# Kernel optimization log

Hardware: AMD Instinct MI355X
Metric: run time of the kernel (lower is better)

Reference implementation:

```python
import jax, jax.numpy as jnp
import numpy as np

B, N, M, D = 32, 1024, 256, 512
NEG_INF = -1e9  # keras Softmax mask additive constant


def _length_mask(key, batch, length):
    # realistic padding masks: first L positions valid, L >= length//4
    lens = jax.random.randint(key, (batch,), length // 4, length + 1)
    return jnp.arange(length)[None, :] < lens[:, None]


def setup_inputs() -> dict:
    key = jax.random.key(0)
    k1, k2, k3, k4, k5 = jax.random.split(key, 5)
    context = jax.random.normal(k1, (B, N, D), dtype=jnp.float32)
    query = jax.random.normal(k2, (B, M, D), dtype=jnp.float32)
    c_mask = _length_mask(k3, B, N)
    q_mask = _length_mask(k4, B, M)
    # Dense(units=1, use_bias=False) kernel over concat([q, c, q*c]) -> (3D, 1)
    w = jax.random.normal(k5, (3 * D, 1), dtype=jnp.float32) * (1.0 / np.sqrt(3 * D))
    return {"context": context, "query": query, "c_mask": c_mask, "q_mask": q_mask, "w": w}


def reference(context, query, c_mask, q_mask, w):
    d = context.shape[-1]
    # stack order in original: [q_matrix, c_matrix, q*c]
    w_q = w[:d, 0]
    w_c = w[d:2 * d, 0]
    w_m = w[2 * d:, 0]
    # trilinear similarity S[b,n,m] = q_j.w_q + c_i.w_c + (c_i*q_j).w_m, decomposed
    S = (context @ w_c)[:, :, None] \
        + (query @ w_q)[:, None, :] \
        + jnp.einsum('bnd,bmd->bnm', context * w_m, query)
    # context-direction softmax over query axis (axis=2), masked by q_mask
    A = jax.nn.softmax(jnp.where(q_mask[:, None, :], S, NEG_INF), axis=2)
    # query-direction softmax over context axis (axis=1), masked by c_mask
    Bm = jax.nn.softmax(jnp.where(c_mask[:, :, None], S, NEG_INF), axis=1)
    # context-to-query attention: A @ query -> (b, n, d)
    c2q = jnp.einsum('bnm,bmd->bnd', A, query)
    # query-to-context: (A @ B^T) @ context -> (b, n, d)
    q2c = jnp.einsum('bnk,bjk,bjd->bnd', A, Bm, context)
    out = jnp.concatenate([context, c2q, context * c2q, context * q2c], axis=-1)
    return out
```

## Files before the change

### kernel.cpp

```cpp
#include <hip/hip_runtime.h>
#include <hip/hip_bf16.h>

#define B_ 32
#define N_ 1024
#define M_ 256
#define D_ 512

typedef __attribute__((ext_vector_type(8))) short short8;
typedef __attribute__((ext_vector_type(4))) float f32x4;

#define OFF_S     ((size_t)0)
#define OFF_CTXW  ((size_t)8388608)
#define OFF_ANM   ((size_t)8388608)
#define OFF_BMT   ((size_t)12582912)
#define OFF_QB    ((size_t)16777216)
#define OFF_QT    ((size_t)18874368)
#define OFF_CT    ((size_t)20971520)
#define OFF_CDOT  ((size_t)29360128)
#define OFF_QDOT  ((size_t)29392896)
#define OFF_RMAX  ((size_t)29401088)
#define OFF_RSUM  ((size_t)29433856)
#define OFF_CMAX  ((size_t)29466624)
#define OFF_CSUM  ((size_t)29474816)
#define OFF_PMAX  ((size_t)29483008)
#define OFF_PSUM  ((size_t)29614080)
#define OFF_RPMAX ((size_t)29745152)
#define OFF_RPSUM ((size_t)29876224)

__global__ __launch_bounds__(256) void prep_ctx(
    const float* __restrict__ ctx, const float* __restrict__ w,
    __hip_bfloat16* __restrict__ ctxw, __hip_bfloat16* __restrict__ cT,
    float* __restrict__ cdot)
{
    __shared__ float t[64][65];
    int b = blockIdx.z, n0 = blockIdx.y * 64, d0 = blockIdx.x * 64;
    int tr = threadIdx.x >> 6, tc = threadIdx.x & 63;
    const float* sp = ctx + ((size_t)b * N_ + n0) * D_ + d0;
    __hip_bfloat16* cwp = ctxw + ((size_t)b * N_ + n0) * D_ + d0;
    float wmv = w[2 * D_ + d0 + tc];
    float wcv = w[D_ + d0 + tc];
#pragma unroll
    for (int i = 0; i < 16; ++i) {
        int r = tr + i * 4;
        float x = sp[(size_t)r * D_ + tc];
        t[r][tc] = x;
        cwp[(size_t)r * D_ + tc] = __float2bfloat16(x * wmv);
        float p = x * wcv;
#pragma unroll
        for (int off = 32; off; off >>= 1) p += __shfl_down(p, off, 64);
        if (tc == 0) atomicAdd(cdot + b * N_ + n0 + r, p);
    }
    __syncthreads();
    __hip_bfloat16* dp = cT + ((size_t)b * D_ + d0) * N_ + n0;
#pragma unroll
    for (int i = 0; i < 16; ++i)
        dp[(size_t)(tr + i * 4) * N_ + tc] = __float2bfloat16(t[tc][tr + i * 4]);
}

__global__ __launch_bounds__(256) void prep_q(
    const float* __restrict__ qry, const float* __restrict__ w,
    __hip_bfloat16* __restrict__ qb, __hip_bfloat16* __restrict__ qT,
    float* __restrict__ qdot)
{
    __shared__ float t[64][65];
    int b = blockIdx.z, m0 = blockIdx.y * 64, d0 = blockIdx.x * 64;
    int tr = threadIdx.x >> 6, tc = threadIdx.x & 63;
    const float* sp = qry + ((size_t)b * M_ + m0) * D_ + d0;
    __hip_bfloat16* qbp = qb + ((size_t)b * M_ + m0) * D_ + d0;
    float wqv = w[d0 + tc];
#pragma unroll
    for (int i = 0; i < 16; ++i) {
        int r = tr + i * 4;
        float x = sp[(size_t)r * D_ + tc];
        t[r][tc] = x;
        qbp[(size_t)r * D_ + tc] = __float2bfloat16(x);
        float p = x * wqv;
#pragma unroll
        for (int off = 32; off; off >>= 1) p += __shfl_down(p, off, 64);
        if (tc == 0) atomicAdd(qdot + b * M_ + m0 + r, p);
    }
    __syncthreads();
    __hip_bfloat16* dp = qT + ((size_t)b * D_ + d0) * M_ + m0;
#pragma unroll
    for (int i = 0; i < 16; ++i)
        dp[(size_t)(tr + i * 4) * M_ + tc] = __float2bfloat16(t[tc][tr + i * 4]);
}


__device__ __forceinline__ void gl2lds16(const __hip_bfloat16* g, __hip_bfloat16* l) {
    __builtin_amdgcn_global_load_lds(
        (const __attribute__((address_space(1))) unsigned int*)g,
        (__attribute__((address_space(3))) unsigned int*)l, 16, 0, 0);
}

template<int KTOT>
__device__ __forceinline__ void mfma128(
    const __hip_bfloat16* __restrict__ Abase, int lda,
    const __hip_bfloat16* __restrict__ Bbase, int ldb,
    __hip_bfloat16* As, __hip_bfloat16* Bs, f32x4 acc[4][4])
{
    const int tid = threadIdx.x;
    const int w = tid >> 6, lane = tid & 63;
    const int quad = lane >> 4, lr = lane & 15;
    const int wr = w >> 1, wc = w & 1;
    const int srow = w * 32 + (lane >> 2);
    const int scol = (lane & 3) * 8;
    const __hip_bfloat16* ga0 = Abase + (size_t)srow * lda + scol;
    const __hip_bfloat16* ga1 = ga0 + (size_t)16 * lda;
    const __hip_bfloat16* gb0 = Bbase + (size_t)srow * ldb + scol;
    const __hip_bfloat16* gb1 = gb0 + (size_t)16 * ldb;
    __hip_bfloat16* la0 = As + w * 1024;
    __hip_bfloat16* la1 = As + w * 1024 + 512;
    __hip_bfloat16* lb0 = Bs + w * 1024;
    __hip_bfloat16* lb1 = Bs + w * 1024 + 512;
    const int aoff = (wr * 64 + lr) * 32 + quad * 8;
    const int boff = (wc * 64 + lr) * 32 + quad * 8;

    for (int k0 = 0; k0 < KTOT; k0 += 32) {
        gl2lds16(ga0, la0); gl2lds16(ga1, la1);
        gl2lds16(gb0, lb0); gl2lds16(gb1, lb1);
        ga0 += 32; ga1 += 32; gb0 += 32; gb1 += 32;
        asm volatile("s_waitcnt vmcnt(0)" ::: "memory");
        __syncthreads();
        short8 a[4], bb[4];
        const short8* ap = (const short8*)(As + aoff);
        const short8* bp = (const short8*)(Bs + boff);
#pragma unroll
        for (int fi = 0; fi < 4; ++fi) a[fi] = ap[fi * 64];
#pragma unroll
        for (int fj = 0; fj < 4; ++fj) bb[fj] = bp[fj * 64];
#pragma unroll
        for (int fi = 0; fi < 4; ++fi)
#pragma unroll
            for (int fj = 0; fj < 4; ++fj)
                acc[fi][fj] = __builtin_amdgcn_mfma_f32_16x16x32_bf16(
                    a[fi], bb[fj], acc[fi][fj], 0, 0, 0);
        __syncthreads();
    }
}

template<int KTOT>
__device__ __forceinline__ void mfma128x2(
    const __hip_bfloat16* __restrict__ Abase, int lda,
    const __hip_bfloat16* __restrict__ B1base,
    const __hip_bfloat16* __restrict__ B2base, int ldb,
    __hip_bfloat16* As, __hip_bfloat16* B1s, __hip_bfloat16* B2s,
    f32x4 acc1[4][4], f32x4 acc2[4][4])
{
    const int tid = threadIdx.x;
    const int w = tid >> 6, lane = tid & 63;
    const int quad = lane >> 4, lr = lane & 15;
    const int wr = w >> 1, wc = w & 1;
    const int srow = w * 32 + (lane >> 2);
    const int scol = (lane & 3) * 8;
    const __hip_bfloat16* ga0 = Abase + (size_t)srow * lda + scol;
    const __hip_bfloat16* ga1 = ga0 + (size_t)16 * lda;
    const __hip_bfloat16* gb10 = B1base + (size_t)srow * ldb + scol;
    const __hip_bfloat16* gb11 = gb10 + (size_t)16 * ldb;
    const __hip_bfloat16* gb20 = B2base + (size_t)srow * ldb + scol;
    const __hip_bfloat16* gb21 = gb20 + (size_t)16 * ldb;
    __hip_bfloat16* la0 = As + w * 1024;
    __hip_bfloat16* la1 = la0 + 512;
    __hip_bfloat16* lb10 = B1s + w * 1024;
    __hip_bfloat16* lb11 = lb10 + 512;
    __hip_bfloat16* lb20 = B2s + w * 1024;
    __hip_bfloat16* lb21 = lb20 + 512;
    const int aoff = (wr * 64 + lr) * 32 + quad * 8;
    const int boff = (wc * 64 + lr) * 32 + quad * 8;

    for (int k0 = 0; k0 < KTOT; k0 += 32) {
        gl2lds16(ga0, la0); gl2lds16(ga1, la1);
        gl2lds16(gb10, lb10); gl2lds16(gb11, lb11);
        gl2lds16(gb20, lb20); gl2lds16(gb21, lb21);
        ga0 += 32; ga1 += 32; gb10 += 32; gb11 += 32; gb20 += 32; gb21 += 32;
        asm volatile("s_waitcnt vmcnt(0)" ::: "memory");
        __syncthreads();
        short8 a[4], b1[4], b2[4];
        const short8* ap = (const short8*)(As + aoff);
        const short8* bp1 = (const short8*)(B1s + boff);
        const short8* bp2 = (const short8*)(B2s + boff);
#pragma unroll
        for (int fi = 0; fi < 4; ++fi) a[fi] = ap[fi * 64];
#pragma unroll
        for (int fj = 0; fj < 4; ++fj) { b1[fj] = bp1[fj * 64]; b2[fj] = bp2[fj * 64]; }
#pragma unroll
        for (int fi = 0; fi < 4; ++fi)
#pragma unroll
            for (int fj = 0; fj < 4; ++fj) {
                acc1[fi][fj] = __builtin_amdgcn_mfma_f32_16x16x32_bf16(
                    a[fi], b1[fj], acc1[fi][fj], 0, 0, 0);
                acc2[fi][fj] = __builtin_amdgcn_mfma_f32_16x16x32_bf16(
                    a[fi], b2[fj], acc2[fi][fj], 0, 0, 0);
            }
        __syncthreads();
    }
}

#define ACC_INIT(acc) \
    _Pragma("unroll") for (int i_ = 0; i_ < 4; ++i_) \
    _Pragma("unroll") for (int j_ = 0; j_ < 4; ++j_) acc[i_][j_] = (f32x4){0.f, 0.f, 0.f, 0.f};

#define EPI_IDX const int tid = threadIdx.x, lane = tid & 63, quad = lane >> 4, lr = lane & 15; \
    const int wr = tid >> 7, wc = (tid >> 6) & 1;

__global__ __launch_bounds__(256) void s_gemm_stats(
    const __hip_bfloat16* __restrict__ ctxw, const __hip_bfloat16* __restrict__ qryb,
    const float* __restrict__ cdot, const float* __restrict__ qdot,
    const int* __restrict__ q_mask, const int* __restrict__ c_mask,
    float* __restrict__ S,
    float* __restrict__ rpmax, float* __restrict__ rpsum,
    float* __restrict__ pmax, float* __restrict__ psum)
{
    __shared__ __align__(16) __hip_bfloat16 As[4096], Bs[4096];
    const int b = blockIdx.z, n0 = blockIdx.y * 128, m0 = blockIdx.x * 128;
    f32x4 acc[4][4];
    ACC_INIT(acc)
    mfma128<512>(ctxw + ((size_t)b * N_ + n0) * D_, D_,
                 qryb + ((size_t)b * M_ + m0) * D_, D_, As, Bs, acc);
    EPI_IDX
    float cd[4][4]; int cmv[4][4];
#pragma unroll
    for (int fi = 0; fi < 4; ++fi)
#pragma unroll
        for (int r = 0; r < 4; ++r) {
            int n = n0 + wr * 64 + fi * 16 + quad * 4 + r;
            cd[fi][r] = cdot[b * N_ + n];
            cmv[fi][r] = c_mask[b * N_ + n];
        }
    float qd[4]; int qmv[4];
#pragma unroll
    for (int fj = 0; fj < 4; ++fj) {
        int m = m0 + wc * 64 + fj * 16 + lr;
        qd[fj] = qdot[b * M_ + m];
        qmv[fj] = q_mask[b * M_ + m];
    }
#pragma unroll
    for (int fi = 0; fi < 4; ++fi)
#pragma unroll
        for (int r = 0; r < 4; ++r) {
            int n = n0 + wr * 64 + fi * 16 + quad * 4 + r;
            size_t rowoff = ((size_t)b * N_ + n) * M_;
#pragma unroll
            for (int fj = 0; fj < 4; ++fj) {
                int m = m0 + wc * 64 + fj * 16 + lr;
                S[rowoff + m] = acc[fi][fj][r] + cd[fi][r] + qd[fj];
            }
        }
    const int part = blockIdx.x * 2 + wc;
#pragma unroll
    for (int fi = 0; fi < 4; ++fi)
#pragma unroll
        for (int r = 0; r < 4; ++r) {
            float xs[4], mx = -1e30f;
#pragma unroll
            for (int fj = 0; fj < 4; ++fj) {
                xs[fj] = qmv[fj] ? (acc[fi][fj][r] + cd[fi][r] + qd[fj]) : -1e9f;
                mx = fmaxf(mx, xs[fj]);
            }
#pragma unroll
            for (int off = 1; off < 16; off <<= 1)
                mx = fmaxf(mx, __shfl_xor(mx, off, 64));
            float se = 0.f;
#pragma unroll
            for (int fj = 0; fj < 4; ++fj) se += __expf(xs[fj] - mx);
#pragma unroll
            for (int off = 1; off < 16; off <<= 1)
                se += __shfl_xor(se, off, 64);
            if (lr == 0) {
                int n = n0 + wr * 64 + fi * 16 + quad * 4 + r;
                rpmax[((size_t)b * N_ + n) * 4 + part] = mx;
                rpsum[((size_t)b * N_ + n) * 4 + part] = se;
            }
        }
    const int ch = blockIdx.y * 2 + wr;
#pragma unroll
    for (int fj = 0; fj < 4; ++fj) {
        float mx = -1e30f;
#pragma unroll
        for (int fi = 0; fi < 4; ++fi)
#pragma unroll
            for (int r = 0; r < 4; ++r) {
                float x = cmv[fi][r] ? (acc[fi][fj][r] + cd[fi][r] + qd[fj]) : -1e9f;
                mx = fmaxf(mx, x);
            }
        mx = fmaxf(mx, __shfl_xor(mx, 16, 64));
        mx = fmaxf(mx, __shfl_xor(mx, 32, 64));
        float se = 0.f;
#pragma unroll
        for (int fi = 0; fi < 4; ++fi)
#pragma unroll
            for (int r = 0; r < 4; ++r) {
                float x = cmv[fi][r] ? (acc[fi][fj][r] + cd[fi][r] + qd[fj]) : -1e9f;
                se += __expf(x - mx);
            }
        se += __shfl_xor(se, 16, 64);
        se += __shfl_xor(se, 32, 64);
        if (lane < 16) {
            int m = m0 + wc * 64 + fj * 16 + lr;
            pmax[((size_t)b * 16 + ch) * M_ + m] = mx;
            psum[((size_t)b * 16 + ch) * M_ + m] = se;
        }
    }
}

__global__ __launch_bounds__(256) void q2cpart_mfma(
    const __hip_bfloat16* __restrict__ ctxT, const __hip_bfloat16* __restrict__ BmT,
    __hip_bfloat16* __restrict__ Q2CT)
{
    __shared__ __align__(16) __hip_bfloat16 As[4096], Bs[4096];
    const int b = blockIdx.z, d0 = blockIdx.y * 128, m0 = blockIdx.x * 128;
    f32x4 acc[4][4];
    ACC_INIT(acc)
    mfma128<1024>(ctxT + ((size_t)b * D_ + d0) * N_, N_,
                  BmT + ((size_t)b * M_ + m0) * N_, N_, As, Bs, acc);
    EPI_IDX
#pragma unroll
    for (int fi = 0; fi < 4; ++fi) {
#pragma unroll
        for (int r = 0; r < 4; ++r) {
            int d = d0 + wr * 64 + fi * 16 + quad * 4 + r;
#pragma unroll
            for (int fj = 0; fj < 4; ++fj) {
                int m = m0 + wc * 64 + fj * 16 + lr;
                Q2CT[((size_t)b * D_ + d) * M_ + m] = __float2bfloat16(acc[fi][fj][r]);
            }
        }
    }
}

__global__ __launch_bounds__(256) void out_fused_mfma(
    const __hip_bfloat16* __restrict__ Anm, const __hip_bfloat16* __restrict__ qryT,
    const __hip_bfloat16* __restrict__ Q2CT, const float* __restrict__ ctx,
    float* __restrict__ out)
{
    __shared__ __align__(16) __hip_bfloat16 As[4096], B1s[4096], B2s[4096];
    const int b = blockIdx.z, n0 = blockIdx.y * 128, d0 = blockIdx.x * 128;
    f32x4 acc1[4][4], acc2[4][4];
    ACC_INIT(acc1)
    ACC_INIT(acc2)
    mfma128x2<256>(Anm + ((size_t)b * N_ + n0) * M_, M_,
                   qryT + ((size_t)b * D_ + d0) * M_,
                   Q2CT + ((size_t)b * D_ + d0) * M_, M_,
                   As, B1s, B2s, acc1, acc2);
    EPI_IDX
#pragma unroll
    for (int fi = 0; fi < 4; ++fi) {
#pragma unroll
        for (int r = 0; r < 4; ++r) {
            int n = n0 + wr * 64 + fi * 16 + quad * 4 + r;
            size_t ibase = ((size_t)b * N_ + n) * D_;
            size_t obase = ((size_t)b * N_ + n) * (4 * D_);
#pragma unroll
            for (int fj = 0; fj < 4; ++fj) {
                int d = d0 + wc * 64 + fj * 16 + lr;
                float c = ctx[ibase + d];
                float v1 = acc1[fi][fj][r];
                float v2 = acc2[fi][fj][r];
                out[obase + d] = c;
                out[obase + D_ + d] = v1;
                out[obase + 2 * D_ + d] = c * v1;
                out[obase + 3 * D_ + d] = c * v2;
            }
        }
    }
}


__global__ __launch_bounds__(256) void combine_stats(
    const float* __restrict__ pmax, const float* __restrict__ psum,
    const float* __restrict__ rpmax, const float* __restrict__ rpsum,
    float* __restrict__ cmax, float* __restrict__ csum,
    float* __restrict__ rmax, float* __restrict__ rsum)
{
    int idx = blockIdx.x * 256 + threadIdx.x;
    if (idx < B_ * M_) {
        int b = idx >> 8, m = idx & 255;
        float mx = -1e30f;
#pragma unroll
        for (int ch = 0; ch < 16; ++ch)
            mx = fmaxf(mx, pmax[((size_t)b * 16 + ch) * M_ + m]);
        float sm = 0.f;
#pragma unroll
        for (int ch = 0; ch < 16; ++ch)
            sm += psum[((size_t)b * 16 + ch) * M_ + m] *
                  __expf(pmax[((size_t)b * 16 + ch) * M_ + m] - mx);
        cmax[idx] = mx; csum[idx] = sm;
    } else {
        int row = idx - B_ * M_;
        float mx = -1e30f;
#pragma unroll
        for (int p = 0; p < 4; ++p)
            mx = fmaxf(mx, rpmax[(size_t)row * 4 + p]);
        float sm = 0.f;
#pragma unroll
        for (int p = 0; p < 4; ++p)
            sm += rpsum[(size_t)row * 4 + p] *
                  __expf(rpmax[(size_t)row * 4 + p] - mx);
        rmax[row] = mx; rsum[row] = sm;
    }
}

__global__ __launch_bounds__(256) void normalize_kernel(
    const float* __restrict__ S, __hip_bfloat16* __restrict__ Anm,
    __hip_bfloat16* __restrict__ BmT,
    const int* __restrict__ q_mask, const int* __restrict__ c_mask,
    const float* __restrict__ rmax, const float* __restrict__ rsum,
    const float* __restrict__ cmax, const float* __restrict__ csum)
{
    __shared__ float t[64][65];
    int b = blockIdx.z, n0 = blockIdx.y * 64, m0 = blockIdx.x * 64;
    int tr = threadIdx.x >> 6, tc = threadIdx.x & 63;
    int m = m0 + tc;
    int qm = q_mask[b * M_ + m];
    float cmx = cmax[b * M_ + m], csm = csum[b * M_ + m];
#pragma unroll
    for (int i = 0; i < 16; ++i) {
        int n = n0 + tr + i * 4;
        size_t idx = ((size_t)b * N_ + n) * M_ + m;
        float s = S[idx];
        float a  = qm ? __expf(s - rmax[b * N_ + n]) / rsum[b * N_ + n] : 0.f;
        float bm = c_mask[b * N_ + n] ? __expf(s - cmx) / csm : 0.f;
        Anm[idx] = __float2bfloat16(a);
        t[tc][tr + i * 4] = bm;
    }
    __syncthreads();
#pragma unroll
    for (int i = 0; i < 16; ++i) {
        int ml = tr + i * 4;
        BmT[((size_t)b * M_ + m0 + ml) * N_ + n0 + tc] = __float2bfloat16(t[ml][tc]);
    }
}

extern "C" void kernel_launch(void* const* d_in, const int* in_sizes, int n_in,
                              void* d_out, int out_size, void* d_ws, size_t ws_size,
                              hipStream_t stream) {
    const float* ctx   = (const float*)d_in[0];
    const float* qry   = (const float*)d_in[1];
    const int*   cmask = (const int*)d_in[2];
    const int*   qmask = (const int*)d_in[3];
    const float* w     = (const float*)d_in[4];
    float* out = (float*)d_out;
    float* ws  = (float*)d_ws;

    float* S = ws + OFF_S;
    __hip_bfloat16* ctxw = (__hip_bfloat16*)(ws + OFF_CTXW);
    __hip_bfloat16* Anm  = (__hip_bfloat16*)(ws + OFF_ANM);
    __hip_bfloat16* BmT  = (__hip_bfloat16*)(ws + OFF_BMT);
    __hip_bfloat16* qb   = (__hip_bfloat16*)(ws + OFF_QB);
    __hip_bfloat16* Q2CT = (__hip_bfloat16*)(ws + OFF_QB);
    __hip_bfloat16* qT   = (__hip_bfloat16*)(ws + OFF_QT);
    __hip_bfloat16* cT   = (__hip_bfloat16*)(ws + OFF_CT);
    float* cdot = ws + OFF_CDOT;
    float* qdot = ws + OFF_QDOT;
    float* rmax = ws + OFF_RMAX;
    float* rsum = ws + OFF_RSUM;
    float* cmx  = ws + OFF_CMAX;
    float* csm  = ws + OFF_CSUM;
    float* pmax = ws + OFF_PMAX;
    float* psum = ws + OFF_PSUM;
    float* rpmax = ws + OFF_RPMAX;
    float* rpsum = ws + OFF_RPSUM;

    hipMemsetAsync(cdot, 0, (size_t)(B_ * N_ + B_ * M_) * sizeof(float), stream);

    dim3 gpc(D_ / 64, N_ / 64, B_);
    prep_ctx<<<gpc, 256, 0, stream>>>(ctx, w, ctxw, cT, cdot);
    dim3 gpq(D_ / 64, M_ / 64, B_);
    prep_q<<<gpq, 256, 0, stream>>>(qry, w, qb, qT, qdot);

    dim3 gS(M_ / 128, N_ / 128, B_);
    s_gemm_stats<<<gS, 256, 0, stream>>>(ctxw, qb, cdot, qdot, qmask, cmask,
                                         S, rpmax, rpsum, pmax, psum);

    combine_stats<<<(B_ * M_ + B_ * N_) / 256, 256, 0, stream>>>(
        pmax, psum, rpmax, rpsum, cmx, csm, rmax, rsum);

    dim3 gN(M_ / 64, N_ / 64, B_);
    normalize_kernel<<<gN, 256, 0, stream>>>(S, Anm, BmT, qmask, cmask,
                                             rmax, rsum, cmx, csm);

    dim3 gP(M_ / 128, D_ / 128, B_);
    q2cpart_mfma<<<gP, 256, 0, stream>>>(cT, BmT, Q2CT);

    dim3 gO(D_ / 128, N_ / 128, B_);
    out_fused_mfma<<<gO, 256, 0, stream>>>(Anm, qT, Q2CT, ctx, out);
}
```

Measured before the change: 504.8 us.

## Double-buffer LDS tiles in MFMA GEMM loops and merge prep kernels

The shared MFMA GEMM helpers now keep two LDS stages. The next K-slice is issued with global_load_lds while the current slice is consumed, which removes one barrier per iteration and the explicit vmcnt wait. This is meant to hide global-load latency behind MFMA work. The cost is double the LDS per block (48KB in the fused output kernel), which may lower occupancy. The context and query prep kernels are also merged into one launch using an extended grid, to save a kernel launch and its tail.

```diff
diff --git a/kernel.cpp b/kernel.cpp
--- a/kernel.cpp
+++ b/kernel.cpp
@@ -27,63 +27,57 @@
 #define OFF_RPMAX ((size_t)29745152)
 #define OFF_RPSUM ((size_t)29876224)
 
-__global__ __launch_bounds__(256) void prep_ctx(
-    const float* __restrict__ ctx, const float* __restrict__ w,
+__global__ __launch_bounds__(256) void prep_all(
+    const float* __restrict__ ctx, const float* __restrict__ qry,
+    const float* __restrict__ w,
     __hip_bfloat16* __restrict__ ctxw, __hip_bfloat16* __restrict__ cT,
-    float* __restrict__ cdot)
+    float* __restrict__ cdot,
+    __hip_bfloat16* __restrict__ qb, __hip_bfloat16* __restrict__ qT,
+    float* __restrict__ qdot)
 {
     __shared__ float t[64][65];
-    int b = blockIdx.z, n0 = blockIdx.y * 64, d0 = blockIdx.x * 64;
+    int b = blockIdx.z, d0 = blockIdx.x * 64;
     int tr = threadIdx.x >> 6, tc = threadIdx.x & 63;
-    const float* sp = ctx + ((size_t)b * N_ + n0) * D_ + d0;
-    __hip_bfloat16* cwp = ctxw + ((size_t)b * N_ + n0) * D_ + d0;
-    float wmv = w[2 * D_ + d0 + tc];
-    float wcv = w[D_ + d0 + tc];
+    const float* src;
+    __hip_bfloat16* rowdst;
+    __hip_bfloat16* trdst;
+    float* dotdst;
+    float wrow, wdot;
+    int ldt;
+    if (blockIdx.y < N_ / 64) {
+        int r0 = blockIdx.y * 64;
+        src    = ctx + ((size_t)b * N_ + r0) * D_ + d0;
+        rowdst = ctxw + ((size_t)b * N_ + r0) * D_ + d0;
+        trdst  = cT + ((size_t)b * D_ + d0) * N_ + r0;
+        dotdst = cdot + b * N_ + r0;
+        wrow = w[2 * D_ + d0 + tc];
+        wdot = w[D_ + d0 + tc];
+        ldt = N_;
+    } else {
+        int r0 = (blockIdx.y - N_ / 64) * 64;
+        src    = qry + ((size_t)b * M_ + r0) * D_ + d0;
+        rowdst = qb + ((size_t)b * M_ + r0) * D_ + d0;
+        trdst  = qT + ((size_t)b * D_ + d0) * M_ + r0;
+        dotdst = qdot + b * M_ + r0;
+        wrow = 1.0f;
+        wdot = w[d0 + tc];
+        ldt = M_;
+    }
 #pragma unroll
     for (int i = 0; i < 16; ++i) {
         int r = tr + i * 4;
-        float x = sp[(size_t)r * D_ + tc];
+        float x = src[(size_t)r * D_ + tc];
         t[r][tc] = x;
-        cwp[(size_t)r * D_ + tc] = __float2bfloat16(x * wmv);
-        float p = x * wcv;
+        rowdst[(size_t)r * D_ + tc] = __float2bfloat16(x * wrow);
+        float p = x * wdot;
 #pragma unroll
         for (int off = 32; off; off >>= 1) p += __shfl_down(p, off, 64);
-        if (tc == 0) atomicAdd(cdot + b * N_ + n0 + r, p);
+        if (tc == 0) atomicAdd(dotdst + r, p);
     }
     __syncthreads();
-    __hip_bfloat16* dp = cT + ((size_t)b * D_ + d0) * N_ + n0;
 #pragma unroll
     for (int i = 0; i < 16; ++i)
-        dp[(size_t)(tr + i * 4) * N_ + tc] = __float2bfloat16(t[tc][tr + i * 4]);
-}
-
-__global__ __launch_bounds__(256) void prep_q(
-    const float* __restrict__ qry, const float* __restrict__ w,
-    __hip_bfloat16* __restrict__ qb, __hip_bfloat16* __restrict__ qT,
-    float* __restrict__ qdot)
-{
-    __shared__ float t[64][65];
-    int b = blockIdx.z, m0 = blockIdx.y * 64, d0 = blockIdx.x * 64;
-    int tr = threadIdx.x >> 6, tc = threadIdx.x & 63;
-    const float* sp = qry + ((size_t)b * M_ + m0) * D_ + d0;
-    __hip_bfloat16* qbp = qb + ((size_t)b * M_ + m0) * D_ + d0;
-    float wqv = w[d0 + tc];
-#pragma unroll
-    for (int i = 0; i < 16; ++i) {
-        int r = tr + i * 4;
-        float x = sp[(size_t)r * D_ + tc];
-        t[r][tc] = x;
-        qbp[(size_t)r * D_ + tc] = __float2bfloat16(x);
-        float p = x * wqv;
-#pragma unroll
-        for (int off = 32; off; off >>= 1) p += __shfl_down(p, off, 64);
-        if (tc == 0) atomicAdd(qdot + b * M_ + m0 + r, p);
-    }
-    __syncthreads();
-    __hip_bfloat16* dp = qT + ((size_t)b * D_ + d0) * M_ + m0;
-#pragma unroll
-    for (int i = 0; i < 16; ++i)
-        dp[(size_t)(tr + i * 4) * M_ + tc] = __float2bfloat16(t[tc][tr + i * 4]);
+        trdst[(size_t)(tr + i * 4) * ldt + tc] = __float2bfloat16(t[tc][tr + i * 4]);
 }
 
 
@@ -109,22 +103,27 @@
     const __hip_bfloat16* ga1 = ga0 + (size_t)16 * lda;
     const __hip_bfloat16* gb0 = Bbase + (size_t)srow * ldb + scol;
     const __hip_bfloat16* gb1 = gb0 + (size_t)16 * ldb;
-    __hip_bfloat16* la0 = As + w * 1024;
-    __hip_bfloat16* la1 = As + w * 1024 + 512;
-    __hip_bfloat16* lb0 = Bs + w * 1024;
-    __hip_bfloat16* lb1 = Bs + w * 1024 + 512;
+    const int lws = w * 1024;
     const int aoff = (wr * 64 + lr) * 32 + quad * 8;
     const int boff = (wc * 64 + lr) * 32 + quad * 8;
 
+    gl2lds16(ga0, As + lws); gl2lds16(ga1, As + lws + 512);
+    gl2lds16(gb0, Bs + lws); gl2lds16(gb1, Bs + lws + 512);
+    __syncthreads();
+
+    int cur = 0;
     for (int k0 = 0; k0 < KTOT; k0 += 32) {
-        gl2lds16(ga0, la0); gl2lds16(ga1, la1);
-        gl2lds16(gb0, lb0); gl2lds16(gb1, lb1);
-        ga0 += 32; ga1 += 32; gb0 += 32; gb1 += 32;
-        asm volatile("s_waitcnt vmcnt(0)" ::: "memory");
-        __syncthreads();
+        const bool more = (k0 + 32 < KTOT);
+        if (more) {
+            const int nb = (cur ^ 1) << 12;
+            gl2lds16(ga0 + 32, As + nb + lws); gl2lds16(ga1 + 32, As + nb + lws + 512);
+            gl2lds16(gb0 + 32, Bs + nb + lws); gl2lds16(gb1 + 32, Bs + nb + lws + 512);
+            ga0 += 32; ga1 += 32; gb0 += 32; gb1 += 32;
+        }
+        const int cb = cur << 12;
         short8 a[4], bb[4];
-        const short8* ap = (const short8*)(As + aoff);
-        const short8* bp = (const short8*)(Bs + boff);
+        const short8* ap = (const short8*)(As + cb + aoff);
+        const short8* bp = (const short8*)(Bs + cb + boff);
 #pragma unroll
         for (int fi = 0; fi < 4; ++fi) a[fi] = ap[fi * 64];
 #pragma unroll
@@ -135,7 +134,7 @@
             for (int fj = 0; fj < 4; ++fj)
                 acc[fi][fj] = __builtin_amdgcn_mfma_f32_16x16x32_bf16(
                     a[fi], bb[fj], acc[fi][fj], 0, 0, 0);
-        __syncthreads();
+        if (more) { __syncthreads(); cur ^= 1; }
     }
 }
 
@@ -159,26 +158,30 @@
     const __hip_bfloat16* gb11 = gb10 + (size_t)16 * ldb;
     const __hip_bfloat16* gb20 = B2base + (size_t)srow * ldb + scol;
     const __hip_bfloat16* gb21 = gb20 + (size_t)16 * ldb;
-    __hip_bfloat16* la0 = As + w * 1024;
-    __hip_bfloat16* la1 = la0 + 512;
-    __hip_bfloat16* lb10 = B1s + w * 1024;
-    __hip_bfloat16* lb11 = lb10 + 512;
-    __hip_bfloat16* lb20 = B2s + w * 1024;
-    __hip_bfloat16* lb21 = lb20 + 512;
+    const int lws = w * 1024;
     const int aoff = (wr * 64 + lr) * 32 + quad * 8;
     const int boff = (wc * 64 + lr) * 32 + quad * 8;
 
+    gl2lds16(ga0, As + lws);  gl2lds16(ga1, As + lws + 512);
+    gl2lds16(gb10, B1s + lws); gl2lds16(gb11, B1s + lws + 512);
+    gl2lds16(gb20, B2s + lws); gl2lds16(gb21, B2s + lws + 512);
+    __syncthreads();
+
+    int cur = 0;
     for (int k0 = 0; k0 < KTOT; k0 += 32) {
-        gl2lds16(ga0, la0); gl2lds16(ga1, la1);
-        gl2lds16(gb10, lb10); gl2lds16(gb11, lb11);
-        gl2lds16(gb20, lb20); gl2lds16(gb21, lb21);
-        ga0 += 32; ga1 += 32; gb10 += 32; gb11 += 32; gb20 += 32; gb21 += 32;
-        asm volatile("s_waitcnt vmcnt(0)" ::: "memory");
-        __syncthreads();
+        const bool more = (k0 + 32 < KTOT);
+        if (more) {
+            const int nb = (cur ^ 1) << 12;
+            gl2lds16(ga0 + 32, As + nb + lws);   gl2lds16(ga1 + 32, As + nb + lws + 512);
+            gl2lds16(gb10 + 32, B1s + nb + lws); gl2lds16(gb11 + 32, B1s + nb + lws + 512);
+            gl2lds16(gb20 + 32, B2s + nb + lws); gl2lds16(gb21 + 32, B2s + nb + lws + 512);
+            ga0 += 32; ga1 += 32; gb10 += 32; gb11 += 32; gb20 += 32; gb21 += 32;
+        }
+        const int cb = cur << 12;
         short8 a[4], b1[4], b2[4];
-        const short8* ap = (const short8*)(As + aoff);
-        const short8* bp1 = (const short8*)(B1s + boff);
-        const short8* bp2 = (const short8*)(B2s + boff);
+        const short8* ap = (const short8*)(As + cb + aoff);
+        const short8* bp1 = (const short8*)(B1s + cb + boff);
+        const short8* bp2 = (const short8*)(B2s + cb + boff);
 #pragma unroll
         for (int fi = 0; fi < 4; ++fi) a[fi] = ap[fi * 64];
 #pragma unroll
@@ -192,7 +195,7 @@
                 acc2[fi][fj] = __builtin_amdgcn_mfma_f32_16x16x32_bf16(
                     a[fi], b2[fj], acc2[fi][fj], 0, 0, 0);
             }
-        __syncthreads();
+        if (more) { __syncthreads(); cur ^= 1; }
     }
 }
 
@@ -211,7 +214,7 @@
     float* __restrict__ rpmax, float* __restrict__ rpsum,
     float* __restrict__ pmax, float* __restrict__ psum)
 {
-    __shared__ __align__(16) __hip_bfloat16 As[4096], Bs[4096];
+    __shared__ __align__(16) __hip_bfloat16 As[8192], Bs[8192];
     const int b = blockIdx.z, n0 = blockIdx.y * 128, m0 = blockIdx.x * 128;
     f32x4 acc[4][4];
     ACC_INIT(acc)
@@ -307,7 +310,7 @@
     const __hip_bfloat16* __restrict__ ctxT, const __hip_bfloat16* __restrict__ BmT,
     __hip_bfloat16* __restrict__ Q2CT)
 {
-    __shared__ __align__(16) __hip_bfloat16 As[4096], Bs[4096];
+    __shared__ __align__(16) __hip_bfloat16 As[8192], Bs[8192];
     const int b = blockIdx.z, d0 = blockIdx.y * 128, m0 = blockIdx.x * 128;
     f32x4 acc[4][4];
     ACC_INIT(acc)
@@ -333,7 +336,7 @@
     const __hip_bfloat16* __restrict__ Q2CT, const float* __restrict__ ctx,
     float* __restrict__ out)
 {
-    __shared__ __align__(16) __hip_bfloat16 As[4096], B1s[4096], B2s[4096];
+    __shared__ __align__(16) __hip_bfloat16 As[8192], B1s[8192], B2s[8192];
     const int b = blockIdx.z, n0 = blockIdx.y * 128, d0 = blockIdx.x * 128;
     f32x4 acc1[4][4], acc2[4][4];
     ACC_INIT(acc1)
@@ -463,10 +466,8 @@
 
     hipMemsetAsync(cdot, 0, (size_t)(B_ * N_ + B_ * M_) * sizeof(float), stream);
 
-    dim3 gpc(D_ / 64, N_ / 64, B_);
-    prep_ctx<<<gpc, 256, 0, stream>>>(ctx, w, ctxw, cT, cdot);
-    dim3 gpq(D_ / 64, M_ / 64, B_);
-    prep_q<<<gpq, 256, 0, stream>>>(qry, w, qb, qT, qdot);
+    dim3 gp(D_ / 64, (N_ + M_) / 64, B_);
+    prep_all<<<gp, 256, 0, stream>>>(ctx, qry, w, ctxw, cT, cdot, qb, qT, qdot);
 
     dim3 gS(M_ / 128, N_ / 128, B_);
     s_gemm_stats<<<gS, 256, 0, stream>>>(ctxw, qb, cdot, qdot, qmask, cmask,
```

Result: no change. 514.7 us (+2.0%).

## Merge prep kernels, fold stat combining into normalize, vectorize memory access

Applied to the files above, without the earlier changes.

Merges the context and query prep kernels into a single launch, and removes the separate combine_stats kernel by recomputing the per-column and per-row softmax statistics inside each normalize block. Both kernels now use float4 loads, vectorized bf16 stores, and 16-element short8 writes for the transposed outputs. The aim is fewer launches and wider, better-coalesced global accesses. In exchange, every normalize block redundantly recomputes statistics for its tile, and division is replaced by a reciprocal multiply.

```diff
diff --git a/kernel.cpp b/kernel.cpp
--- a/kernel.cpp
+++ b/kernel.cpp
@@ -18,72 +18,74 @@
 #define OFF_CT    ((size_t)20971520)
 #define OFF_CDOT  ((size_t)29360128)
 #define OFF_QDOT  ((size_t)29392896)
-#define OFF_RMAX  ((size_t)29401088)
-#define OFF_RSUM  ((size_t)29433856)
-#define OFF_CMAX  ((size_t)29466624)
-#define OFF_CSUM  ((size_t)29474816)
 #define OFF_PMAX  ((size_t)29483008)
 #define OFF_PSUM  ((size_t)29614080)
 #define OFF_RPMAX ((size_t)29745152)
 #define OFF_RPSUM ((size_t)29876224)
 
-__global__ __launch_bounds__(256) void prep_ctx(
-    const float* __restrict__ ctx, const float* __restrict__ w,
+__global__ __launch_bounds__(256) void prep_all(
+    const float* __restrict__ ctx, const float* __restrict__ qry,
+    const float* __restrict__ w,
     __hip_bfloat16* __restrict__ ctxw, __hip_bfloat16* __restrict__ cT,
-    float* __restrict__ cdot)
-{
-    __shared__ float t[64][65];
-    int b = blockIdx.z, n0 = blockIdx.y * 64, d0 = blockIdx.x * 64;
-    int tr = threadIdx.x >> 6, tc = threadIdx.x & 63;
-    const float* sp = ctx + ((size_t)b * N_ + n0) * D_ + d0;
-    __hip_bfloat16* cwp = ctxw + ((size_t)b * N_ + n0) * D_ + d0;
-    float wmv = w[2 * D_ + d0 + tc];
-    float wcv = w[D_ + d0 + tc];
-#pragma unroll
-    for (int i = 0; i < 16; ++i) {
-        int r = tr + i * 4;
-        float x = sp[(size_t)r * D_ + tc];
-        t[r][tc] = x;
-        cwp[(size_t)r * D_ + tc] = __float2bfloat16(x * wmv);
-        float p = x * wcv;
-#pragma unroll
-        for (int off = 32; off; off >>= 1) p += __shfl_down(p, off, 64);
-        if (tc == 0) atomicAdd(cdot + b * N_ + n0 + r, p);
-    }
-    __syncthreads();
-    __hip_bfloat16* dp = cT + ((size_t)b * D_ + d0) * N_ + n0;
-#pragma unroll
-    for (int i = 0; i < 16; ++i)
-        dp[(size_t)(tr + i * 4) * N_ + tc] = __float2bfloat16(t[tc][tr + i * 4]);
-}
-
-__global__ __launch_bounds__(256) void prep_q(
-    const float* __restrict__ qry, const float* __restrict__ w,
+    float* __restrict__ cdot,
     __hip_bfloat16* __restrict__ qb, __hip_bfloat16* __restrict__ qT,
     float* __restrict__ qdot)
 {
     __shared__ float t[64][65];
-    int b = blockIdx.z, m0 = blockIdx.y * 64, d0 = blockIdx.x * 64;
-    int tr = threadIdx.x >> 6, tc = threadIdx.x & 63;
-    const float* sp = qry + ((size_t)b * M_ + m0) * D_ + d0;
-    __hip_bfloat16* qbp = qb + ((size_t)b * M_ + m0) * D_ + d0;
-    float wqv = w[d0 + tc];
-#pragma unroll
-    for (int i = 0; i < 16; ++i) {
-        int r = tr + i * 4;
-        float x = sp[(size_t)r * D_ + tc];
-        t[r][tc] = x;
-        qbp[(size_t)r * D_ + tc] = __float2bfloat16(x);
-        float p = x * wqv;
-#pragma unroll
-        for (int off = 32; off; off >>= 1) p += __shfl_down(p, off, 64);
-        if (tc == 0) atomicAdd(qdot + b * M_ + m0 + r, p);
+    const int b = blockIdx.z, d0 = blockIdx.x * 64;
+    const int tid = threadIdx.x;
+    const float* src;
+    __hip_bfloat16* rowdst;
+    __hip_bfloat16* trdst;
+    float* dotdst;
+    int ldt;
+    float4 wmv, wdv;
+    const int lr16 = tid & 15, rband = tid >> 4;
+    const int c = lr16 * 4;
+    if (blockIdx.y < N_ / 64) {
+        int r0 = blockIdx.y * 64;
+        src    = ctx + ((size_t)b * N_ + r0) * D_ + d0;
+        rowdst = ctxw + ((size_t)b * N_ + r0) * D_ + d0;
+        trdst  = cT + ((size_t)b * D_ + d0) * N_ + r0;
+        dotdst = cdot + b * N_ + r0;
+        wmv = *(const float4*)(w + 2 * D_ + d0 + c);
+        wdv = *(const float4*)(w + D_ + d0 + c);
+        ldt = N_;
+    } else {
+        int r0 = (blockIdx.y - N_ / 64) * 64;
+        src    = qry + ((size_t)b * M_ + r0) * D_ + d0;
+        rowdst = qb + ((size_t)b * M_ + r0) * D_ + d0;
+        trdst  = qT + ((size_t)b * D_ + d0) * M_ + r0;
+        dotdst = qdot + b * M_ + r0;
+        wmv = (float4){1.f, 1.f, 1.f, 1.f};
+        wdv = *(const float4*)(w + d0 + c);
+        ldt = M_;
+    }
+#pragma unroll
+    for (int i = 0; i < 4; ++i) {
+        int r = i * 16 + rband;
+        float4 x = *(const float4*)(src + (size_t)r * D_ + c);
+        t[r][c] = x.x; t[r][c + 1] = x.y; t[r][c + 2] = x.z; t[r][c + 3] = x.w;
+        __hip_bfloat16 o[4] __attribute__((aligned(8)));
+        o[0] = __float2bfloat16(x.x * wmv.x);
+        o[1] = __float2bfloat16(x.y * wmv.y);
+        o[2] = __float2bfloat16(x.z * wmv.z);
+        o[3] = __float2bfloat16(x.w * wmv.w);
+        *(ushort4*)(rowdst + (size_t)r * D_ + c) = *(ushort4*)o;
+        float p = x.x * wdv.x + x.y * wdv.y + x.z * wdv.z + x.w * wdv.w;
+#pragma unroll
+        for (int off = 1; off < 16; off <<= 1) p += __shfl_xor(p, off, 64);
+        if (lr16 == 0) atomicAdd(dotdst + r, p);
     }
     __syncthreads();
-    __hip_bfloat16* dp = qT + ((size_t)b * D_ + d0) * M_ + m0;
-#pragma unroll
-    for (int i = 0; i < 16; ++i)
-        dp[(size_t)(tr + i * 4) * M_ + tc] = __float2bfloat16(t[tc][tr + i * 4]);
+    const int dr = tid >> 2, sseg = tid & 3;
+    __hip_bfloat16 o[16] __attribute__((aligned(16)));
+#pragma unroll
+    for (int j = 0; j < 16; ++j)
+        o[j] = __float2bfloat16(t[sseg * 16 + j][dr]);
+    __hip_bfloat16* dp = trdst + (size_t)dr * ldt + sseg * 16;
+    ((short8*)dp)[0] = ((short8*)o)[0];
+    ((short8*)dp)[1] = ((short8*)o)[1];
 }
 
 
@@ -365,70 +367,76 @@
     }
 }
 
-
-__global__ __launch_bounds__(256) void combine_stats(
-    const float* __restrict__ pmax, const float* __restrict__ psum,
-    const float* __restrict__ rpmax, const float* __restrict__ rpsum,
-    float* __restrict__ cmax, float* __restrict__ csum,
-    float* __restrict__ rmax, float* __restrict__ rsum)
-{
-    int idx = blockIdx.x * 256 + threadIdx.x;
-    if (idx < B_ * M_) {
-        int b = idx >> 8, m = idx & 255;
-        float mx = -1e30f;
-#pragma unroll
-        for (int ch = 0; ch < 16; ++ch)
-            mx = fmaxf(mx, pmax[((size_t)b * 16 + ch) * M_ + m]);
-        float sm = 0.f;
-#pragma unroll
-        for (int ch = 0; ch < 16; ++ch)
-            sm += psum[((size_t)b * 16 + ch) * M_ + m] *
-                  __expf(pmax[((size_t)b * 16 + ch) * M_ + m] - mx);
-        cmax[idx] = mx; csum[idx] = sm;
-    } else {
-        int row = idx - B_ * M_;
-        float mx = -1e30f;
-#pragma unroll
-        for (int p = 0; p < 4; ++p)
-            mx = fmaxf(mx, rpmax[(size_t)row * 4 + p]);
-        float sm = 0.f;
-#pragma unroll
-        for (int p = 0; p < 4; ++p)
-            sm += rpsum[(size_t)row * 4 + p] *
-                  __expf(rpmax[(size_t)row * 4 + p] - mx);
-        rmax[row] = mx; rsum[row] = sm;
-    }
-}
-
 __global__ __launch_bounds__(256) void normalize_kernel(
     const float* __restrict__ S, __hip_bfloat16* __restrict__ Anm,
     __hip_bfloat16* __restrict__ BmT,
     const int* __restrict__ q_mask, const int* __restrict__ c_mask,
-    const float* __restrict__ rmax, const float* __restrict__ rsum,
-    const float* __restrict__ cmax, const float* __restrict__ csum)
+    const float* __restrict__ pmax, const float* __restrict__ psum,
+    const float* __restrict__ rpmax, const float* __restrict__ rpsum)
 {
     __shared__ float t[64][65];
-    int b = blockIdx.z, n0 = blockIdx.y * 64, m0 = blockIdx.x * 64;
-    int tr = threadIdx.x >> 6, tc = threadIdx.x & 63;
-    int m = m0 + tc;
-    int qm = q_mask[b * M_ + m];
-    float cmx = cmax[b * M_ + m], csm = csum[b * M_ + m];
-#pragma unroll
-    for (int i = 0; i < 16; ++i) {
-        int n = n0 + tr + i * 4;
-        size_t idx = ((size_t)b * N_ + n) * M_ + m;
-        float s = S[idx];
-        float a  = qm ? __expf(s - rmax[b * N_ + n]) / rsum[b * N_ + n] : 0.f;
-        float bm = c_mask[b * N_ + n] ? __expf(s - cmx) / csm : 0.f;
-        Anm[idx] = __float2bfloat16(a);
-        t[tc][tr + i * 4] = bm;
+    __shared__ float cmx_s[64], cinv_s[64], rmx_s[64], rinv_s[64];
+    const int b = blockIdx.z, n0 = blockIdx.y * 64, m0 = blockIdx.x * 64;
+    const int tid = threadIdx.x;
+    if (tid < 64) {
+        int m = m0 + tid;
+        float mx = -1e30f;
+#pragma unroll
+        for (int ch = 0; ch < 16; ++ch)
+            mx = fmaxf(mx, pmax[((size_t)b * 16 + ch) * M_ + m]);
+        float sm = 0.f;
+#pragma unroll
+        for (int ch = 0; ch < 16; ++ch)
+            sm += psum[((size_t)b * 16 + ch) * M_ + m] *
+                  __expf(pmax[((size_t)b * 16 + ch) * M_ + m] - mx);
+        cmx_s[tid] = mx; cinv_s[tid] = 1.0f / sm;
+    } else if (tid < 128) {
+        int rl = tid - 64;
+        size_t row = (size_t)b * N_ + n0 + rl;
+        float mx = -1e30f;
+#pragma unroll
+        for (int p = 0; p < 4; ++p)
+            mx = fmaxf(mx, rpmax[row * 4 + p]);
+        float sm = 0.f;
+#pragma unroll
+        for (int p = 0; p < 4; ++p)
+            sm += rpsum[row * 4 + p] * __expf(rpmax[row * 4 + p] - mx);
+        rmx_s[rl] = mx; rinv_s[rl] = 1.0f / sm;
     }
     __syncthreads();
-#pragma unroll
-    for (int i = 0; i < 16; ++i) {
-        int ml = tr + i * 4;
-        BmT[((size_t)b * M_ + m0 + ml) * N_ + n0 + tc] = __float2bfloat16(t[ml][tc]);
-    }
+    const int lr16 = tid & 15, rband = tid >> 4;
+    const int c = lr16 * 4;
+    int4 qm4 = *(const int4*)(q_mask + b * M_ + m0 + c);
+    float cmx0 = cmx_s[c], cmx1 = cmx_s[c + 1], cmx2 = cmx_s[c + 2], cmx3 = cmx_s[c + 3];
+    float ci0 = cinv_s[c], ci1 = cinv_s[c + 1], ci2 = cinv_s[c + 2], ci3 = cinv_s[c + 3];
+#pragma unroll
+    for (int i = 0; i < 4; ++i) {
+        int r = i * 16 + rband;
+        int n = n0 + r;
+        int cm = c_mask[b * N_ + n];
+        float rmx = rmx_s[r], rinv = rinv_s[r];
+        size_t idx = ((size_t)b * N_ + n) * M_ + m0 + c;
+        float4 s4 = *(const float4*)(S + idx);
+        __hip_bfloat16 av[4] __attribute__((aligned(8)));
+        av[0] = __float2bfloat16(qm4.x ? __expf(s4.x - rmx) * rinv : 0.f);
+        av[1] = __float2bfloat16(qm4.y ? __expf(s4.y - rmx) * rinv : 0.f);
+        av[2] = __float2bfloat16(qm4.z ? __expf(s4.z - rmx) * rinv : 0.f);
+        av[3] = __float2bfloat16(qm4.w ? __expf(s4.w - rmx) * rinv : 0.f);
+        *(ushort4*)(Anm + idx) = *(ushort4*)av;
+        t[r][c]     = cm ? __expf(s4.x - cmx0) * ci0 : 0.f;
+        t[r][c + 1] = cm ? __expf(s4.y - cmx1) * ci1 : 0.f;
+        t[r][c + 2] = cm ? __expf(s4.z - cmx2) * ci2 : 0.f;
+        t[r][c + 3] = cm ? __expf(s4.w - cmx3) * ci3 : 0.f;
+    }
+    __syncthreads();
+    const int mr = tid >> 2, sseg = tid & 3;
+    __hip_bfloat16 o[16] __attribute__((aligned(16)));
+#pragma unroll
+    for (int j = 0; j < 16; ++j)
+        o[j] = __float2bfloat16(t[sseg * 16 + j][mr]);
+    __hip_bfloat16* dp = BmT + ((size_t)b * M_ + m0 + mr) * N_ + n0 + sseg * 16;
+    ((short8*)dp)[0] = ((short8*)o)[0];
+    ((short8*)dp)[1] = ((short8*)o)[1];
 }
 
 extern "C" void kernel_launch(void* const* d_in, const int* in_sizes, int n_in,
@@ -452,10 +460,6 @@
     __hip_bfloat16* cT   = (__hip_bfloat16*)(ws + OFF_CT);
     float* cdot = ws + OFF_CDOT;
     float* qdot = ws + OFF_QDOT;
-    float* rmax = ws + OFF_RMAX;
-    float* rsum = ws + OFF_RSUM;
-    float* cmx  = ws + OFF_CMAX;
-    float* csm  = ws + OFF_CSUM;
     float* pmax = ws + OFF_PMAX;
     float* psum = ws + OFF_PSUM;
     float* rpmax = ws + OFF_RPMAX;
@@ -463,21 +467,16 @@
 
     hipMemsetAsync(cdot, 0, (size_t)(B_ * N_ + B_ * M_) * sizeof(float), stream);
 
-    dim3 gpc(D_ / 64, N_ / 64, B_);
-    prep_ctx<<<gpc, 256, 0, stream>>>(ctx, w, ctxw, cT, cdot);
-    dim3 gpq(D_ / 64, M_ / 64, B_);
-    prep_q<<<gpq, 256, 0, stream>>>(qry, w, qb, qT, qdot);
+    dim3 gp(D_ / 64, (N_ + M_) / 64, B_);
+    prep_all<<<gp, 256, 0, stream>>>(ctx, qry, w, ctxw, cT, cdot, qb, qT, qdot);
 
     dim3 gS(M_ / 128, N_ / 128, B_);
     s_gemm_stats<<<gS, 256, 0, stream>>>(ctxw, qb, cdot, qdot, qmask, cmask,
                                          S, rpmax, rpsum, pmax, psum);
 
-    combine_stats<<<(B_ * M_ + B_ * N_) / 256, 256, 0, stream>>>(
-        pmax, psum, rpmax, rpsum, cmx, csm, rmax, rsum);
-
     dim3 gN(M_ / 64, N_ / 64, B_);
     normalize_kernel<<<gN, 256, 0, stream>>>(S, Anm, BmT, qmask, cmask,
-                                             rmax, rsum, cmx, csm);
+                                             pmax, psum, rpmax, rpsum);
 
     dim3 gP(M_ / 128, D_ / 128, B_);
     q2cpart_mfma<<<gP, 256, 0, stream>>>(cT, BmT, Q2CT);
```

Measured after the change: 482.0 us. 1.05x faster.
